# Optimization experiments

Hardware: AMD Instinct MI355X
Metric: run time of the kernel (lower is better)

## Reference

```python
import jax, jax.numpy as jnp
import numpy as np


def _maxpool2(x):
    # 2x2 max pool, stride 2, on NCHW
    b, c, h, w = x.shape
    return x.reshape(b, c, h // 2, 2, w // 2, 2).max(axis=(3, 5))


def _conv1x1(w, x):
    # w: [out_c, in_c], x: [B, in_c, H, W]
    return jnp.einsum('oc,bchw->bohw', w, x)


def setup_inputs() -> dict:
    key = jax.random.key(0)
    ks = jax.random.split(key, 5)
    B, C, H, W = 16, 64, 64, 64
    x = jax.random.normal(ks[0], (B, C, H, W), dtype=jnp.float32)
    # 1x1 conv weights (spectral-norm treated as already-normalized params)
    Wt = jax.random.normal(ks[1], (C // 8, C), dtype=jnp.float32) * 0.05
    Wp = jax.random.normal(ks[2], (C // 8, C), dtype=jnp.float32) * 0.05
    Wg = jax.random.normal(ks[3], (C // 2, C), dtype=jnp.float32) * 0.05
    Wo = jax.random.normal(ks[4], (C, C // 2), dtype=jnp.float32) * 0.05
    gamma = jnp.float32(0.5)  # nonzero so attention branch contributes
    return {"x": x, "Wt": Wt, "Wp": Wp, "Wg": Wg, "Wo": Wo, "gamma": gamma}


def reference(x, Wt, Wp, Wg, Wo, gamma):
    b, c, h, w = x.shape
    theta = _conv1x1(Wt, x).reshape(b, c // 8, h * w)            # [B, C/8, HW]
    phi = _maxpool2(_conv1x1(Wp, x)).reshape(b, c // 8, -1)      # [B, C/8, HW/4]
    g = _maxpool2(_conv1x1(Wg, x)).reshape(b, c // 2, -1)        # [B, C/2, HW/4]
    # scores: [B, HW, HW/4]; softmax over pooled (key) axis
    beta = jax.nn.softmax(jnp.einsum('bct,bcs->bts', theta, phi), axis=-1)
    o = jnp.einsum('bcs,bts->bct', g, beta).reshape(b, c // 2, h, w)
    o = _conv1x1(Wo, o)                                          # [B, C, H, W]
    return gamma * o + x
```

## Files before the change

### kernel.cpp

```cpp
#include <hip/hip_runtime.h>
#include <math.h>

#define NB   16
#define NC   64
#define HWs  4096
#define NPS  1024
#define LOG2E 1.44269504088896341f

static constexpr size_t PHI_OFF = (size_t)NB * HWs * 8;
static constexpr size_t GT_OFF  = PHI_OFF + (size_t)NB * NPS * 8;

typedef short s16x8 __attribute__((ext_vector_type(8)));
typedef float f32x4 __attribute__((ext_vector_type(4)));

#define LD8G(p) (*(const s16x8*)(p))

__device__ inline unsigned short f2bf(float f) {
    unsigned int u = __float_as_uint(f);
    u += 0x7fffu + ((u >> 16) & 1u);
    return (unsigned short)(u >> 16);
}
__device__ inline unsigned int pk2(float a, float b) {
    unsigned int ua = __float_as_uint(a); ua += 0x7fffu + ((ua >> 16) & 1u);
    unsigned int ub = __float_as_uint(b); ub += 0x7fffu + ((ub >> 16) & 1u);
    return (ua >> 16) | (ub & 0xffff0000u);
}

__global__ __launch_bounds__(256) void k_proj(
    const float* __restrict__ x, const float* __restrict__ Wt,
    const float* __restrict__ Wp, const float* __restrict__ Wg,
    unsigned short* __restrict__ ws)
{
    __shared__ float xs[64 * 128];

    unsigned short* theta = ws;
    unsigned short* phi   = ws + PHI_OFF;
    unsigned short* gT    = ws + GT_OFF;

    const int tid = threadIdx.x;
    const int blk = blockIdx.x;
    const int b   = blk >> 5;
    const int rp  = blk & 31;

    const float* xsrc = x + (size_t)b * NC * HWs + rp * 128;
#pragma unroll
    for (int i = 0; i < 8; ++i) {
        const int idx = i * 256 + tid;
        const int ci  = idx >> 5;
        const int f4  = idx & 31;
        float4 v = *(const float4*)(xsrc + (size_t)ci * HWs + f4 * 4);
        *(float4*)(xs + ci * 128 + f4 * 4) = v;
    }
    __syncthreads();

    const int h    = tid & 127;
    const int half = __builtin_amdgcn_readfirstlane(tid >> 7);
    const int row  = h & 1;
    const int col  = h >> 1;
    const int px   = row * 64 + col;

    float a8[8], ag[16];
#pragma unroll
    for (int j = 0; j < 8; ++j)  a8[j] = 0.f;
#pragma unroll
    for (int j = 0; j < 16; ++j) ag[j] = 0.f;

    const float* W8 = half ? Wp : Wt;
    const float* WG = Wg + half * 16 * NC;

#pragma unroll 4
    for (int ci = 0; ci < NC; ++ci) {
        const float xv = xs[ci * 128 + px];
#pragma unroll
        for (int j = 0; j < 8; ++j)  a8[j] += W8[j * NC + ci] * xv;
#pragma unroll
        for (int j = 0; j < 16; ++j) ag[j] += WG[j * NC + ci] * xv;
    }

    if (half == 0) {
        const int q = (2 * rp + row) * 64 + col;
        uint4 pkd;
        pkd.x = pk2(a8[0] * LOG2E, a8[1] * LOG2E);
        pkd.y = pk2(a8[2] * LOG2E, a8[3] * LOG2E);
        pkd.z = pk2(a8[4] * LOG2E, a8[5] * LOG2E);
        pkd.w = pk2(a8[6] * LOG2E, a8[7] * LOG2E);
        *(uint4*)(theta + ((size_t)b * HWs + q) * 8) = pkd;
    }

#pragma unroll
    for (int j = 0; j < 8; ++j) {
        float v = a8[j];
        v = fmaxf(v, __shfl_xor(v, 1));
        v = fmaxf(v, __shfl_xor(v, 2));
        a8[j] = v;
    }
#pragma unroll
    for (int j = 0; j < 16; ++j) {
        float v = ag[j];
        v = fmaxf(v, __shfl_xor(v, 1));
        v = fmaxf(v, __shfl_xor(v, 2));
        ag[j] = v;
    }

    if ((h & 3) == 0) {
        const int ps = rp * 32 + (h >> 2);
        if (half == 1) {
            uint4 pkd;
            pkd.x = pk2(a8[0], a8[1]); pkd.y = pk2(a8[2], a8[3]);
            pkd.z = pk2(a8[4], a8[5]); pkd.w = pk2(a8[6], a8[7]);
            *(uint4*)(phi + ((size_t)b * NPS + ps) * 8) = pkd;
        }
#pragma unroll
        for (int j = 0; j < 16; ++j) {
            const int c = half * 16 + j;
            gT[((size_t)b * 32 + c) * NPS + ps] = f2bf(ag[j]);
        }
    }
}

__global__ __launch_bounds__(256) void k_attn(
    const float* __restrict__ x, const float* __restrict__ Wo,
    const float* __restrict__ gamma_p, const unsigned short* __restrict__ ws,
    float* __restrict__ out)
{
    __shared__ __align__(16) unsigned char smem[18432];

    const int tid  = threadIdx.x;
    const int wave = __builtin_amdgcn_readfirstlane(tid >> 6);
    const int lane = tid & 63;
    const int quad = lane >> 4, lr = lane & 15;
    const int blk  = blockIdx.x;
    const int b    = blk >> 6;
    const int q0   = (blk & 63) * 64;

    const unsigned short* th = ws + (size_t)b * HWs * 8;
    const unsigned short* ph = ws + PHI_OFF + (size_t)b * NPS * 8;
    const unsigned short* gp = ws + GT_OFF + (size_t)b * 32 * NPS;
    unsigned short* Pw = (unsigned short*)smem + wave * 2304;

    const s16x8 zf = {0, 0, 0, 0, 0, 0, 0, 0};

    const s16x8 thA = (quad == 0) ? LD8G(th + (size_t)(q0 + wave * 16 + lr) * 8) : zf;

    f32x4 O[2];
    f32x4 l4;
#pragma unroll
    for (int r = 0; r < 4; ++r) { O[0][r] = 0.f; O[1][r] = 0.f; l4[r] = 0.f; }

    s16x8 phB_c[4], phB_n[4];
    s16x8 Gf_c[2][2], Gf_n[2][2];
#pragma unroll
    for (int ss = 0; ss < 4; ++ss)
        phB_c[ss] = (quad == 0) ? LD8G(ph + (size_t)(ss * 16 + lr) * 8) : zf;

    for (int t = 0; t < 16; ++t) {
        const int s0 = t * 64;
        const int sn = (t < 15 ? t + 1 : 15) * 64;

#pragma unroll
        for (int ss = 0; ss < 4; ++ss)
            phB_n[ss] = (quad == 0) ? LD8G(ph + (size_t)(sn + ss * 16 + lr) * 8) : zf;
#pragma unroll
        for (int kc = 0; kc < 2; ++kc)
#pragma unroll
            for (int cs = 0; cs < 2; ++cs)
                Gf_n[kc][cs] = LD8G(gp + (size_t)(cs * 16 + lr) * NPS + s0 + kc * 32 + quad * 8);

        const f32x4 zc = {0.f, 0.f, 0.f, 0.f};
        f32x4 S[4];
#pragma unroll
        for (int ss = 0; ss < 4; ++ss)
            S[ss] = __builtin_amdgcn_mfma_f32_16x16x32_bf16(thA, phB_c[ss], zc, 0, 0, 0);

        if (t > 0) {
            const unsigned short* Pb = Pw + ((t - 1) & 1) * 1152;
#pragma unroll
            for (int kc = 0; kc < 2; ++kc) {
                const s16x8 Pf = *(const s16x8*)(Pb + lr * 72 + kc * 32 + quad * 8);
#pragma unroll
                for (int cs = 0; cs < 2; ++cs)
                    O[cs] = __builtin_amdgcn_mfma_f32_16x16x32_bf16(Pf, Gf_c[kc][cs], O[cs], 0, 0, 0);
            }
        }

        unsigned short* Pbw = Pw + (t & 1) * 1152;
#pragma unroll
        for (int ss = 0; ss < 4; ++ss)
#pragma unroll
            for (int r = 0; r < 4; ++r) {
                const float p = exp2f(S[ss][r]);
                l4[r] += p;
                Pbw[(quad * 4 + r) * 72 + ss * 16 + lr] =
                    (unsigned short)(__float_as_uint(p) >> 16);
            }

#pragma unroll
        for (int ss = 0; ss < 4; ++ss) phB_c[ss] = phB_n[ss];
#pragma unroll
        for (int kc = 0; kc < 2; ++kc)
#pragma unroll
            for (int cs = 0; cs < 2; ++cs) Gf_c[kc][cs] = Gf_n[kc][cs];
    }

    {
        const unsigned short* Pb = Pw + (15 & 1) * 1152;
#pragma unroll
        for (int kc = 0; kc < 2; ++kc) {
            const s16x8 Pf = *(const s16x8*)(Pb + lr * 72 + kc * 32 + quad * 8);
#pragma unroll
            for (int cs = 0; cs < 2; ++cs)
                O[cs] = __builtin_amdgcn_mfma_f32_16x16x32_bf16(Pf, Gf_c[kc][cs], O[cs], 0, 0, 0);
        }
    }

#pragma unroll
    for (int r = 0; r < 4; ++r) {
        float v = l4[r];
        v += __shfl_xor(v, 1);
        v += __shfl_xor(v, 2);
        v += __shfl_xor(v, 4);
        v += __shfl_xor(v, 8);
        l4[r] = 1.f / v;
    }

    __syncthreads();
    float* otile = (float*)smem;
#pragma unroll
    for (int cs = 0; cs < 2; ++cs) {
        f32x4 v;
#pragma unroll
        for (int r = 0; r < 4; ++r) v[r] = O[cs][r] * l4[r];
        *(f32x4*)(otile + (cs * 16 + lr) * 68 + wave * 16 + quad * 4) = v;
    }
    __syncthreads();

    const int qq = tid & 63;
    const int quarter = __builtin_amdgcn_readfirstlane(tid >> 6);
    float acc[16];
#pragma unroll
    for (int j = 0; j < 16; ++j) acc[j] = 0.f;
    for (int c = 0; c < 32; ++c) {
        const float ov = otile[c * 68 + qq];
#pragma unroll
        for (int j = 0; j < 16; ++j)
            acc[j] += Wo[(quarter * 16 + j) * 32 + c] * ov;
    }
    const float gam = gamma_p[0];
#pragma unroll
    for (int j = 0; j < 16; ++j) {
        const size_t a = ((size_t)b * NC + quarter * 16 + j) * HWs + q0 + qq;
        out[a] = gam * acc[j] + x[a];
    }
}

extern "C" void kernel_launch(void* const* d_in, const int* in_sizes, int n_in,
                              void* d_out, int out_size, void* d_ws, size_t ws_size,
                              hipStream_t stream) {
    const float* x     = (const float*)d_in[0];
    const float* Wt    = (const float*)d_in[1];
    const float* Wp    = (const float*)d_in[2];
    const float* Wg    = (const float*)d_in[3];
    const float* Wo    = (const float*)d_in[4];
    const float* gamma = (const float*)d_in[5];
    float* out = (float*)d_out;
    unsigned short* ws = (unsigned short*)d_ws;

    k_proj<<<512, 256, 0, stream>>>(x, Wt, Wp, Wg, ws);
    k_attn<<<1024, 256, 0, stream>>>(x, Wo, gamma, ws, out);
}
```

Before: 132.9 us.

## Split attention key range across two wave groups per block and merge partials

```diff
diff --git a/kernel.cpp b/kernel.cpp
--- a/kernel.cpp
+++ b/kernel.cpp
@@ -118,29 +118,32 @@
     }
 }
 
-__global__ __launch_bounds__(256) void k_attn(
+__global__ __launch_bounds__(512, 8) void k_attn(
     const float* __restrict__ x, const float* __restrict__ Wo,
     const float* __restrict__ gamma_p, const unsigned short* __restrict__ ws,
     float* __restrict__ out)
 {
-    __shared__ __align__(16) unsigned char smem[18432];
+    __shared__ __align__(16) unsigned char smem[36864];
 
     const int tid  = threadIdx.x;
     const int wave = __builtin_amdgcn_readfirstlane(tid >> 6);
+    const int qw   = wave & 3;
+    const int sh   = wave >> 2;
     const int lane = tid & 63;
     const int quad = lane >> 4, lr = lane & 15;
     const int blk  = blockIdx.x;
     const int b    = blk >> 6;
     const int q0   = (blk & 63) * 64;
+    const int sBase = sh * 512;
 
     const unsigned short* th = ws + (size_t)b * HWs * 8;
-    const unsigned short* ph = ws + PHI_OFF + (size_t)b * NPS * 8;
-    const unsigned short* gp = ws + GT_OFF + (size_t)b * 32 * NPS;
+    const unsigned short* ph = ws + PHI_OFF + (size_t)b * NPS * 8 + (size_t)sBase * 8;
+    const unsigned short* gp = ws + GT_OFF + (size_t)b * 32 * NPS + sBase;
     unsigned short* Pw = (unsigned short*)smem + wave * 2304;
 
     const s16x8 zf = {0, 0, 0, 0, 0, 0, 0, 0};
 
-    const s16x8 thA = (quad == 0) ? LD8G(th + (size_t)(q0 + wave * 16 + lr) * 8) : zf;
+    const s16x8 thA = (quad == 0) ? LD8G(th + (size_t)(q0 + qw * 16 + lr) * 8) : zf;
 
     f32x4 O[2];
     f32x4 l4;
@@ -153,9 +156,9 @@
     for (int ss = 0; ss < 4; ++ss)
         phB_c[ss] = (quad == 0) ? LD8G(ph + (size_t)(ss * 16 + lr) * 8) : zf;
 
-    for (int t = 0; t < 16; ++t) {
+    for (int t = 0; t < 8; ++t) {
         const int s0 = t * 64;
-        const int sn = (t < 15 ? t + 1 : 15) * 64;
+        const int sn = (t < 7 ? t + 1 : 7) * 64;
 
 #pragma unroll
         for (int ss = 0; ss < 4; ++ss)
@@ -203,7 +206,7 @@
     }
 
     {
-        const unsigned short* Pb = Pw + (15 & 1) * 1152;
+        const unsigned short* Pb = Pw + (7 & 1) * 1152;
 #pragma unroll
         for (int kc = 0; kc < 2; ++kc) {
             const s16x8 Pf = *(const s16x8*)(Pb + lr * 72 + kc * 32 + quad * 8);
@@ -220,35 +223,59 @@
         v += __shfl_xor(v, 2);
         v += __shfl_xor(v, 4);
         v += __shfl_xor(v, 8);
-        l4[r] = 1.f / v;
-    }
-
-    __syncthreads();
-    float* otile = (float*)smem;
-#pragma unroll
-    for (int cs = 0; cs < 2; ++cs) {
-        f32x4 v;
-#pragma unroll
-        for (int r = 0; r < 4; ++r) v[r] = O[cs][r] * l4[r];
-        *(f32x4*)(otile + (cs * 16 + lr) * 68 + wave * 16 + quad * 4) = v;
+        l4[r] = v;
+    }
+
+    __syncthreads();
+    float* xO    = (float*)smem;
+    float* xl    = xO + 2048;
+    float* otile = xl + 64;
+
+    if (sh == 1) {
+#pragma unroll
+        for (int cs = 0; cs < 2; ++cs) {
+            f32x4 v;
+#pragma unroll
+            for (int r = 0; r < 4; ++r) v[r] = O[cs][r];
+            *(f32x4*)(xO + qw * 512 + (cs * 16 + lr) * 16 + quad * 4) = v;
+        }
+        if (lr == 0) {
+#pragma unroll
+            for (int r = 0; r < 4; ++r) xl[qw * 16 + quad * 4 + r] = l4[r];
+        }
+    }
+    __syncthreads();
+    if (sh == 0) {
+        f32x4 rl;
+#pragma unroll
+        for (int r = 0; r < 4; ++r)
+            rl[r] = 1.f / (l4[r] + xl[qw * 16 + quad * 4 + r]);
+#pragma unroll
+        for (int cs = 0; cs < 2; ++cs) {
+            const f32x4 xv = *(const f32x4*)(xO + qw * 512 + (cs * 16 + lr) * 16 + quad * 4);
+            f32x4 v;
+#pragma unroll
+            for (int r = 0; r < 4; ++r) v[r] = (O[cs][r] + xv[r]) * rl[r];
+            *(f32x4*)(otile + (cs * 16 + lr) * 68 + qw * 16 + quad * 4) = v;
+        }
     }
     __syncthreads();
 
     const int qq = tid & 63;
-    const int quarter = __builtin_amdgcn_readfirstlane(tid >> 6);
-    float acc[16];
-#pragma unroll
-    for (int j = 0; j < 16; ++j) acc[j] = 0.f;
+    const int ocg = wave;
+    float acc[8];
+#pragma unroll
+    for (int j = 0; j < 8; ++j) acc[j] = 0.f;
     for (int c = 0; c < 32; ++c) {
         const float ov = otile[c * 68 + qq];
 #pragma unroll
-        for (int j = 0; j < 16; ++j)
-            acc[j] += Wo[(quarter * 16 + j) * 32 + c] * ov;
+        for (int j = 0; j < 8; ++j)
+            acc[j] += Wo[(ocg * 8 + j) * 32 + c] * ov;
     }
     const float gam = gamma_p[0];
 #pragma unroll
-    for (int j = 0; j < 16; ++j) {
-        const size_t a = ((size_t)b * NC + quarter * 16 + j) * HWs + q0 + qq;
+    for (int j = 0; j < 8; ++j) {
+        const size_t a = ((size_t)b * NC + ocg * 8 + j) * HWs + q0 + qq;
         out[a] = gam * acc[j] + x[a];
     }
 }
@@ -266,5 +293,5 @@
     unsigned short* ws = (unsigned short*)d_ws;
 
     k_proj<<<512, 256, 0, stream>>>(x, Wt, Wp, Wg, ws);
-    k_attn<<<1024, 256, 0, stream>>>(x, Wo, gamma, ws, out);
-}
+    k_attn<<<1024, 512, 0, stream>>>(x, Wo, gamma, ws, out);
+}
```

Result: slower. 284.9 us (+114.4%).
